# Optimization experiments

Hardware: AMD Instinct MI355X
Metric: run time of the kernel (lower is better)

## Reference

```python
import jax, jax.numpy as jnp
import numpy as np

KS = 5          # kernel_size
D = 2           # spatial dim
DX = 0.01       # region kernel spacing
SCALE = 1.0
NX, NY = 32, 32
N = NX * NY


def _region_kernel():
    # gaussians.region_kernel: KS x KS grid of offsets spaced DX, centered at 0
    off = (jnp.arange(KS, dtype=jnp.float32) - (KS - 1) / 2.0) * DX
    gx, gy = jnp.meshgrid(off, off, indexing='ij')
    return jnp.stack([gx, gy], -1).reshape(-1, D)  # (KS*KS, 2)


def _build_cov(scaling, transform):
    # Cholesky-style parameterization: L lower-triangular with diag=scaling,
    # off-diag=transform; cov = L @ L^T (d=2 closed form)
    s0, s1 = scaling[:, 0], scaling[:, 1]
    t = transform[:, 0]
    c00 = s0 * s0
    c01 = s0 * t
    c11 = t * t + s1 * s1
    return jnp.stack([jnp.stack([c00, c01], -1), jnp.stack([c01, c11], -1)], -2)


def _inv2x2(c):
    det = c[:, 0, 0] * c[:, 1, 1] - c[:, 0, 1] * c[:, 1, 0]
    inv = jnp.stack([jnp.stack([c[:, 1, 1], -c[:, 0, 1]], -1),
                     jnp.stack([-c[:, 1, 0], c[:, 0, 0]], -1)], -2)
    return inv / det[:, None, None]


def setup_inputs() -> dict:
    key = jax.random.key(0)
    ks = jax.random.split(key, 20)
    # Gaussian state: grid means as in __init__
    tx = jnp.linspace(-1.0, 1.0, NX) * SCALE
    ty = jnp.linspace(-1.0, 1.0, NY) * SCALE
    gx, gy = jnp.meshgrid(tx, ty, indexing='ij')
    means = jnp.stack([gx, gy], -1).reshape(-1, D).astype(jnp.float32)
    u = 0.1 * jax.random.normal(ks[0], (N, 1), jnp.float32)
    scaling = jnp.exp(-4.5 + 0.2 * jax.random.normal(ks[1], (N, D), jnp.float32)) * SCALE
    transform = 0.002 * jax.random.normal(ks[2], (N, 1), jnp.float32)
    opacities = 2.0 + 0.1 * jax.random.normal(ks[3], (N,), jnp.float32)
    # network weights (4 heads share the first 3 layer shapes)
    convW = 0.05 * jax.random.normal(ks[4], (4, 50, 3, KS, KS), jnp.float32)
    convb = 0.01 * jax.random.normal(ks[5], (4, 50), jnp.float32)
    embW = 0.3 * jax.random.normal(ks[6], (4, 7, 30), jnp.float32)
    embb = 0.01 * jax.random.normal(ks[7], (4, 30), jnp.float32)
    l1W = 0.1 * jax.random.normal(ks[8], (4, 80, 80), jnp.float32)
    l1b = 0.01 * jax.random.normal(ks[9], (4, 80), jnp.float32)
    outW_sol = 0.1 * jax.random.normal(ks[10], (80, 1), jnp.float32)
    outb_sol = 0.01 * jax.random.normal(ks[11], (1,), jnp.float32)
    outW_trans = 0.1 * jax.random.normal(ks[12], (80, 2), jnp.float32)
    outb_trans = 0.01 * jax.random.normal(ks[13], (2,), jnp.float32)
    outW_scale = 0.1 * jax.random.normal(ks[14], (80, 2), jnp.float32)
    outb_scale = 0.01 * jax.random.normal(ks[15], (2,), jnp.float32)
    outW_tform = 0.1 * jax.random.normal(ks[16], (80, 1), jnp.float32)
    outb_tform = 0.01 * jax.random.normal(ks[17], (1,), jnp.float32)
    return {"means": means, "u": u, "scaling": scaling, "transform": transform,
            "opacities": opacities, "convW": convW, "convb": convb,
            "embW": embW, "embb": embb, "l1W": l1W, "l1b": l1b,
            "outW_sol": outW_sol, "outb_sol": outb_sol,
            "outW_trans": outW_trans, "outb_trans": outb_trans,
            "outW_scale": outW_scale, "outb_scale": outb_scale,
            "outW_tform": outW_tform, "outb_tform": outb_tform}


def reference(means, u, scaling, transform, opacities, convW, convb, embW, embb,
              l1W, l1b, outW_sol, outb_sol, outW_trans, outb_trans,
              outW_scale, outb_scale, outW_tform, outb_tform):
    n = means.shape[0]
    cov = _build_cov(scaling, transform)          # (N,2,2)
    conics = _inv2x2(cov)                         # (N,2,2)

    # --- sampling (torch.no_grad block in original) ---
    kern = _region_kernel()                                        # (25,2)
    samples = (means[:, None, :] + kern[None]).reshape(-1, D)      # (M,2), M=N*25
    bc = jnp.all(jnp.abs(samples) < SCALE, -1).astype(means.dtype)[:, None]
    alpha = jax.nn.sigmoid(opacities)                              # (N,)
    diff = samples[:, None, :] - means[None, :, :]                 # (M,N,2)
    Cq = jnp.einsum('nij,mnj->mni', conics, diff)                  # (M,N,2)
    G = jnp.exp(-0.5 * jnp.einsum('mni,mni->mn', diff, Cq)) * alpha[None, :]  # (M,N)
    u_s = G @ u                                                    # (M,1)
    # DIFFUSION pde_rhs = trace of laplacian: sum_n G * (|C q|^2 - tr(C)) * u_n
    trC = conics[:, 0, 0] + conics[:, 1, 1]
    lap = jnp.einsum('mn,mn,nc->mc', G, (Cq ** 2).sum(-1) - trC[None, :], u)  # (M,1)
    in_samples = jax.lax.stop_gradient(jnp.concatenate([u_s, lap, bc], -1))   # (M,3)

    # (N, 25, 3) -> (N, 3, 5, 5)
    img = in_samples.reshape(n, KS * KS, -1).transpose(0, 2, 1).reshape(n, -1, KS, KS)
    in_params = jnp.concatenate([means, u, scaling, transform, opacities[:, None]], -1)  # (N,7)

    # 4 Networks: conv(5x5 -> 1x1, 50ch) + param embed(7->30) + MLP(80->80->out)
    y = jnp.tanh(jnp.einsum('ncij,kocij->kno', img, convW) + convb[:, None, :])   # (4,N,50)
    e = jnp.tanh(jnp.einsum('nf,kfg->kng', in_params, embW) + embb[:, None, :])   # (4,N,30)
    h = jnp.tanh(jnp.einsum('knf,kfg->kng', jnp.concatenate([y, e], -1), l1W)
                 + l1b[:, None, :])                                               # (4,N,80)

    deltas = h[0] @ outW_sol + outb_sol          # (N,1)
    translation = h[1] @ outW_trans + outb_trans # (N,2)
    dscale = h[2] @ outW_scale + outb_scale      # (N,2)
    dtransform = h[3] @ outW_tform + outb_tform  # (N,1)

    u_new = u + deltas
    means_new = means + translation
    scaling_new = scaling * jnp.exp(dscale)
    transform_new = transform + dtransform
    cov_new = _build_cov(scaling_new, transform_new)
    return (u_new, means_new, scaling_new, transform_new, cov_new)
```

## Files before the change

kernel.cpp:

```cpp
#include <hip/hip_runtime.h>
#include <hip/hip_bf16.h>


#define NG 1024

__device__ __forceinline__ float tanh_fast(float x) {
    return 1.0f - 2.0f / (__expf(2.0f * x) + 1.0f);
}

__global__ __launch_bounds__(256) void k_fused(
    const float* __restrict__ means, const float* __restrict__ u,
    const float* __restrict__ scal, const float* __restrict__ trans,
    const float* __restrict__ opac,
    const float* __restrict__ convW, const float* __restrict__ convb,
    const float* __restrict__ embW,  const float* __restrict__ embb,
    const float* __restrict__ l1W,   const float* __restrict__ l1b,
    const float* __restrict__ oWs,  const float* __restrict__ obs,
    const float* __restrict__ oWt,  const float* __restrict__ obt,
    const float* __restrict__ oWsc, const float* __restrict__ obsc,
    const float* __restrict__ oWtf, const float* __restrict__ obtf,
    float* __restrict__ out)
{
    __shared__ float gcomp[NG * 8];
    __shared__ float pus[2][2][32];
    __shared__ float plap[2][2][32];
    __shared__ float simg[2][80];
    __shared__ float hin[2][4][80];
    __shared__ float hv[2][4][80];
    __shared__ float semb[840];
    __shared__ float sembb[120];
    __shared__ float shead[480];
    __shared__ float sheadb[6];
    __shared__ int   cnt;

    const int t  = threadIdx.x;
    const int n0 = blockIdx.x * 2;

    const float mx0 = means[2*n0],   my0 = means[2*n0+1];
    const float mx1 = means[2*n0+2], my1 = means[2*n0+3];
    const float uu0 = u[n0],     uu1 = u[n0+1];
    const float sc00 = scal[2*n0],   sc01 = scal[2*n0+1];
    const float sc10 = scal[2*n0+2], sc11 = scal[2*n0+3];
    const float tr0 = trans[n0], tr1 = trans[n0+1];
    const float op0 = opac[n0],  op1 = opac[n0+1];

    float wcv[75];
    {
        const float* w = convW + (size_t)(t < 200 ? t : 0) * 75;
        #pragma unroll
        for (int j = 0; j < 75; ++j) wcv[j] = w[j];
    }
    float w1[80];
    {
        int k = t / 80, g = t - (t / 80) * 80;
        const float* w = l1W + (size_t)(k * 80) * 80 + g;
        #pragma unroll
        for (int f = 0; f < 80; ++f) w1[f] = w[f * 80];
    }
    float bcv  = (t < 200) ? convb[t] : 0.0f;
    float b1   = l1b[t];
    float b1k3 = l1b[256 + (t & 63)];

    for (int i = t; i < 840; i += 256) semb[i] = embW[i];
    if (t < 120) sembb[t] = embb[t];
    for (int i = t; i < 480; i += 256) {
        float v = (i < 80) ? oWs[i] : (i < 240) ? oWt[i - 80]
                : (i < 400) ? oWsc[i - 240] : oWtf[i - 400];
        shead[i] = v;
    }
    if (t < 6) sheadb[t] = (t == 0) ? obs[0] : (t < 3) ? obt[t-1]
                         : (t < 5) ? obsc[t-3] : obtf[0];

    const float bxmin = fminf(mx0, mx1) - 0.02f, bxmax = fmaxf(mx0, mx1) + 0.02f;
    const float bymin = fminf(my0, my1) - 0.02f, bymax = fmaxf(my0, my1) + 0.02f;

    if (t == 0) cnt = 0;
    __syncthreads();
    for (int g = t; g < NG; g += 256) {
        float gmx = means[2*g], gmy = means[2*g+1];
        float s0  = scal[2*g],  s1  = scal[2*g+1];
        float tt  = trans[g];
        float c00 = s0*s0, c01 = s0*tt, c11 = tt*tt + s1*s1;
        float r2  = 100.0f * (c00 + c11);
        float ddx = fmaxf(fmaxf(bxmin - gmx, gmx - bxmax), 0.0f);
        float ddy = fmaxf(fmaxf(bymin - gmy, gmy - bymax), 0.0f);
        if (ddx*ddx + ddy*ddy <= r2) {
            float idet = 1.0f / (c00*c11 - c01*c01);
            float A = c11*idet, B = -c01*idet, C = c00*idet;
            float alpha = 1.0f / (1.0f + __expf(-opac[g]));
            int slot = atomicAdd(&cnt, 1);
            float4* dst = (float4*)(gcomp + slot*8);
            dst[0] = make_float4(gmx, gmy, A, B);
            dst[1] = make_float4(C, A + C, alpha * u[g], 0.0f);
        }
    }
    __syncthreads();
    const int nsurv = cnt;

    {
        int w = t >> 6, lane = t & 63;
        int l = w >> 1;
        int hc = ((w & 1) << 1) | (lane >> 5);
        int s  = lane & 31; if (s > 24) s = 24;
        int si = s / 5, sj = s - si * 5;
        float gx = l ? mx1 : mx0, gy = l ? my1 : my0;
        float sx = gx + (float)(si - 2) * 0.01f;
        float sy = gy + (float)(sj - 2) * 0.01f;
        float us = 0.0f, lp = 0.0f;
        #pragma unroll 2
        for (int i = hc; i < nsurv; i += 4) {
            float4 a = *(const float4*)(gcomp + i*8);
            float4 b = *(const float4*)(gcomp + i*8 + 4);
            float dx = sx - a.x, dy = sy - a.y;
            float Cq0 = a.z*dx + a.w*dy;
            float Cq1 = a.w*dx + b.x*dy;
            float q   = dx*Cq0 + dy*Cq1;
            float e   = __expf(-0.5f*q) * b.z;
            us += e;
            lp += e * (Cq0*Cq0 + Cq1*Cq1 - b.y);
        }
        us += __shfl_down(us, 32);
        lp += __shfl_down(lp, 32);
        if ((lane & 31) == s && lane < 32) {
            pus[l][w & 1][s] = us; plap[l][w & 1][s] = lp;
        }
    }
    __syncthreads();

    if (t < 50) {
        int l = t / 25, s = t - l * 25;
        float us = pus[l][0][s] + pus[l][1][s];
        float lp = plap[l][0][s] + plap[l][1][s];
        int si = s / 5, sj = s - si * 5;
        float gx = l ? mx1 : mx0, gy = l ? my1 : my0;
        float sx = gx + (float)(si - 2) * 0.01f;
        float sy = gy + (float)(sj - 2) * 0.01f;
        simg[l][s]      = us;
        simg[l][25 + s] = lp;
        simg[l][50 + s] = (fabsf(sx) < 1.0f && fabsf(sy) < 1.0f) ? 1.0f : 0.0f;
    }
    __syncthreads();

    if (t < 200) {
        float a0 = bcv, a1 = bcv;
        #pragma unroll
        for (int j = 0; j < 75; ++j) {
            a0 += simg[0][j] * wcv[j];
            a1 += simg[1][j] * wcv[j];
        }
        int k = t / 50, o = t - k * 50;
        hin[0][k][o] = tanh_fast(a0);
        hin[1][k][o] = tanh_fast(a1);
    } else {
        for (int idx = t - 200; idx < 240; idx += 56) {
            int l = idx / 120, rem = idx - l * 120;
            int k = rem / 30, g = rem - k * 30;
            float acc = sembb[k * 30 + g];
            #pragma unroll
            for (int f = 0; f < 7; ++f) {
                float in0, in1;
                switch (f) {
                    case 0: in0 = mx0;  in1 = mx1;  break;
                    case 1: in0 = my0;  in1 = my1;  break;
                    case 2: in0 = uu0;  in1 = uu1;  break;
                    case 3: in0 = sc00; in1 = sc10; break;
                    case 4: in0 = sc01; in1 = sc11; break;
                    case 5: in0 = tr0;  in1 = tr1;  break;
                    default: in0 = op0; in1 = op1;  break;
                }
                acc += (l ? in1 : in0) * semb[(k*7 + f)*30 + g];
            }
            hin[l][k][50 + g] = tanh_fast(acc);
        }
    }
    __syncthreads();

    {
        int k = t / 80, g = t - (t / 80) * 80;
        float a0 = b1, a1 = b1;
        #pragma unroll
        for (int f = 0; f < 80; ++f) {
            a0 += hin[0][k][f] * w1[f];
            a1 += hin[1][k][f] * w1[f];
        }
        hv[0][k][g] = tanh_fast(a0);
        hv[1][k][g] = tanh_fast(a1);
    }
    if (t < 64) {
        int g = 16 + t;
        float a0 = b1k3, a1 = b1k3;
        #pragma unroll 8
        for (int f = 0; f < 80; ++f) {
            float w = l1W[(3*80 + f)*80 + g];
            a0 += hin[0][3][f] * w;
            a1 += hin[1][3][f] * w;
        }
        hv[0][3][g] = tanh_fast(a0);
        hv[1][3][g] = tanh_fast(a1);
    }
    __syncthreads();

    if (t < 64) {
        int l = (t / 6) & 1, t6 = t % 6;
        int k, base, stride, j;
        if (t6 == 0)      { k = 0; base = 0;   stride = 1; j = 0; }
        else if (t6 < 3)  { k = 1; base = 80;  stride = 2; j = t6 - 1; }
        else if (t6 < 5)  { k = 2; base = 240; stride = 2; j = t6 - 3; }
        else              { k = 3; base = 400; stride = 1; j = 0; }
        float acc = sheadb[t6];
        #pragma unroll 8
        for (int f = 0; f < 80; ++f)
            acc += hv[l][k][f] * shead[base + f * stride + j];

        int sb = (t / 6) * 6;
        float o0 = __shfl(acc, sb + 0);
        float o1 = __shfl(acc, sb + 1);
        float o2 = __shfl(acc, sb + 2);
        float o3 = __shfl(acc, sb + 3);
        float o4 = __shfl(acc, sb + 4);
        float o5 = __shfl(acc, sb + 5);

        if (t == 0 || t == 6) {
            int n = n0 + (t / 6);
            float uu = t ? uu1 : uu0;
            float s0 = t ? sc10 : sc00, s1 = t ? sc11 : sc01;
            float tr = t ? tr1 : tr0;
            float u_new = uu + o0;
            float mxn = (t ? mx1 : mx0) + o1;
            float myn = (t ? my1 : my0) + o2;
            float s0n = s0 * __expf(o3);
            float s1n = s1 * __expf(o4);
            float tn  = tr + o5;
            float c00 = s0n*s0n, c01 = s0n*tn, c11 = tn*tn + s1n*s1n;
            out[n]              = u_new;
            out[1024 + 2*n]     = mxn;
            out[1024 + 2*n + 1] = myn;
            out[3072 + 2*n]     = s0n;
            out[3072 + 2*n + 1] = s1n;
            out[5120 + n]       = tn;
            out[6144 + 4*n]     = c00;
            out[6144 + 4*n + 1] = c01;
            out[6144 + 4*n + 2] = c01;
            out[6144 + 4*n + 3] = c11;
        }
    }
}

extern "C" void kernel_launch(void* const* d_in, const int* in_sizes, int n_in,
                              void* d_out, int out_size, void* d_ws, size_t ws_size,
                              hipStream_t stream)
{
    k_fused<<<dim3(NG / 2), dim3(256), 0, stream>>>(
        (const float*)d_in[0],  (const float*)d_in[1],  (const float*)d_in[2],
        (const float*)d_in[3],  (const float*)d_in[4],  (const float*)d_in[5],
        (const float*)d_in[6],  (const float*)d_in[7],  (const float*)d_in[8],
        (const float*)d_in[9],  (const float*)d_in[10], (const float*)d_in[11],
        (const float*)d_in[12], (const float*)d_in[13], (const float*)d_in[14],
        (const float*)d_in[15], (const float*)d_in[16], (const float*)d_in[17],
        (const float*)d_in[18], (float*)d_out);
}
```

Baseline: 105.2 us.

## Process four Gaussians per block with float4-packed activations to amortize weight loads

Each block now handles four Gaussians instead of two, so the per-block weight loads (conv and l1 weights into registers, embedding and head weights into shared memory) and the culling pass are shared across more outputs. Intermediate activations are stored as float4 interleaved across the four Gaussians, so each weight register feeds four FMAs per shared load. This halves the grid to 256 blocks, which may reduce occupancy across the many CUs. The enlarged bounding box may also let more neighbours survive culling, and each sample now loops over half as many parallel partitions.

Result: slower. 108.7 us (+3.3%).

```diff
diff --git a/kernel.cpp b/kernel.cpp
--- a/kernel.cpp
+++ b/kernel.cpp
@@ -3,6 +3,7 @@
 
 
 #define NG 1024
+#define GPB 4
 
 __device__ __forceinline__ float tanh_fast(float x) {
     return 1.0f - 2.0f / (__expf(2.0f * x) + 1.0f);
@@ -21,12 +22,13 @@
     const float* __restrict__ oWtf, const float* __restrict__ obtf,
     float* __restrict__ out)
 {
-    __shared__ float gcomp[NG * 8];
-    __shared__ float pus[2][2][32];
-    __shared__ float plap[2][2][32];
-    __shared__ float simg[2][80];
-    __shared__ float hin[2][4][80];
-    __shared__ float hv[2][4][80];
+    __shared__ __align__(16) float gcomp[NG * 8];
+    __shared__ float pus[GPB][32];
+    __shared__ float plap[GPB][32];
+    __shared__ float4 simgv[80];
+    __shared__ float4 hinv[4][80];
+    __shared__ float4 hvv[4 * 81];
+    __shared__ float sparams[GPB][8];
     __shared__ float semb[840];
     __shared__ float sembb[120];
     __shared__ float shead[480];
@@ -34,15 +36,28 @@
     __shared__ int   cnt;
 
     const int t  = threadIdx.x;
-    const int n0 = blockIdx.x * 2;
-
-    const float mx0 = means[2*n0],   my0 = means[2*n0+1];
-    const float mx1 = means[2*n0+2], my1 = means[2*n0+3];
-    const float uu0 = u[n0],     uu1 = u[n0+1];
-    const float sc00 = scal[2*n0],   sc01 = scal[2*n0+1];
-    const float sc10 = scal[2*n0+2], sc11 = scal[2*n0+3];
-    const float tr0 = trans[n0], tr1 = trans[n0+1];
-    const float op0 = opac[n0],  op1 = opac[n0+1];
+    const int n0 = blockIdx.x * GPB;
+
+    const float m0x = means[2*n0+0], m0y = means[2*n0+1];
+    const float m1x = means[2*n0+2], m1y = means[2*n0+3];
+    const float m2x = means[2*n0+4], m2y = means[2*n0+5];
+    const float m3x = means[2*n0+6], m3y = means[2*n0+7];
+
+    if (t < 28) {
+        int l = t / 7, f = t - l * 7;
+        int n = n0 + l;
+        float v;
+        switch (f) {
+            case 0: v = means[2*n];   break;
+            case 1: v = means[2*n+1]; break;
+            case 2: v = u[n];         break;
+            case 3: v = scal[2*n];    break;
+            case 4: v = scal[2*n+1];  break;
+            case 5: v = trans[n];     break;
+            default: v = opac[n];     break;
+        }
+        sparams[l][f] = v;
+    }
 
     float wcv[75];
     {
@@ -71,8 +86,10 @@
     if (t < 6) sheadb[t] = (t == 0) ? obs[0] : (t < 3) ? obt[t-1]
                          : (t < 5) ? obsc[t-3] : obtf[0];
 
-    const float bxmin = fminf(mx0, mx1) - 0.02f, bxmax = fmaxf(mx0, mx1) + 0.02f;
-    const float bymin = fminf(my0, my1) - 0.02f, bymax = fmaxf(my0, my1) + 0.02f;
+    const float bxmin = fminf(fminf(m0x, m1x), fminf(m2x, m3x)) - 0.02f;
+    const float bxmax = fmaxf(fmaxf(m0x, m1x), fmaxf(m2x, m3x)) + 0.02f;
+    const float bymin = fminf(fminf(m0y, m1y), fminf(m2y, m3y)) - 0.02f;
+    const float bymax = fmaxf(fmaxf(m0y, m1y), fmaxf(m2y, m3y)) + 0.02f;
 
     if (t == 0) cnt = 0;
     __syncthreads();
@@ -99,16 +116,16 @@
 
     {
         int w = t >> 6, lane = t & 63;
-        int l = w >> 1;
-        int hc = ((w & 1) << 1) | (lane >> 5);
-        int s  = lane & 31; if (s > 24) s = 24;
+        int h = lane >> 5;
+        int s = lane & 31; if (s > 24) s = 24;
         int si = s / 5, sj = s - si * 5;
-        float gx = l ? mx1 : mx0, gy = l ? my1 : my0;
+        float gx = (w == 0) ? m0x : (w == 1) ? m1x : (w == 2) ? m2x : m3x;
+        float gy = (w == 0) ? m0y : (w == 1) ? m1y : (w == 2) ? m2y : m3y;
         float sx = gx + (float)(si - 2) * 0.01f;
         float sy = gy + (float)(sj - 2) * 0.01f;
         float us = 0.0f, lp = 0.0f;
         #pragma unroll 2
-        for (int i = hc; i < nsurv; i += 4) {
+        for (int i = h; i < nsurv; i += 2) {
             float4 a = *(const float4*)(gcomp + i*8);
             float4 b = *(const float4*)(gcomp + i*8 + 4);
             float dx = sx - a.x, dy = sy - a.y;
@@ -121,98 +138,99 @@
         }
         us += __shfl_down(us, 32);
         lp += __shfl_down(lp, 32);
-        if ((lane & 31) == s && lane < 32) {
-            pus[l][w & 1][s] = us; plap[l][w & 1][s] = lp;
-        }
-    }
-    __syncthreads();
-
-    if (t < 50) {
+        if (lane < 32 && (lane & 31) == s) {
+            pus[w][s] = us; plap[w][s] = lp;
+        }
+    }
+    __syncthreads();
+
+    if (t < 100) {
         int l = t / 25, s = t - l * 25;
-        float us = pus[l][0][s] + pus[l][1][s];
-        float lp = plap[l][0][s] + plap[l][1][s];
+        float us = pus[l][s];
+        float lp = plap[l][s];
         int si = s / 5, sj = s - si * 5;
-        float gx = l ? mx1 : mx0, gy = l ? my1 : my0;
+        float gx = (l == 0) ? m0x : (l == 1) ? m1x : (l == 2) ? m2x : m3x;
+        float gy = (l == 0) ? m0y : (l == 1) ? m1y : (l == 2) ? m2y : m3y;
         float sx = gx + (float)(si - 2) * 0.01f;
         float sy = gy + (float)(sj - 2) * 0.01f;
-        simg[l][s]      = us;
-        simg[l][25 + s] = lp;
-        simg[l][50 + s] = (fabsf(sx) < 1.0f && fabsf(sy) < 1.0f) ? 1.0f : 0.0f;
+        float* sg = (float*)simgv;
+        sg[(s)*4 + l]      = us;
+        sg[(25 + s)*4 + l] = lp;
+        sg[(50 + s)*4 + l] = (fabsf(sx) < 1.0f && fabsf(sy) < 1.0f) ? 1.0f : 0.0f;
     }
     __syncthreads();
 
     if (t < 200) {
-        float a0 = bcv, a1 = bcv;
+        float a0 = bcv, a1 = bcv, a2 = bcv, a3 = bcv;
         #pragma unroll
         for (int j = 0; j < 75; ++j) {
-            a0 += simg[0][j] * wcv[j];
-            a1 += simg[1][j] * wcv[j];
+            float4 v = simgv[j];
+            a0 += v.x * wcv[j];
+            a1 += v.y * wcv[j];
+            a2 += v.z * wcv[j];
+            a3 += v.w * wcv[j];
         }
         int k = t / 50, o = t - k * 50;
-        hin[0][k][o] = tanh_fast(a0);
-        hin[1][k][o] = tanh_fast(a1);
+        hinv[k][o] = make_float4(tanh_fast(a0), tanh_fast(a1),
+                                 tanh_fast(a2), tanh_fast(a3));
     } else {
-        for (int idx = t - 200; idx < 240; idx += 56) {
+        for (int idx = t - 200; idx < 480; idx += 56) {
             int l = idx / 120, rem = idx - l * 120;
             int k = rem / 30, g = rem - k * 30;
             float acc = sembb[k * 30 + g];
             #pragma unroll
-            for (int f = 0; f < 7; ++f) {
-                float in0, in1;
-                switch (f) {
-                    case 0: in0 = mx0;  in1 = mx1;  break;
-                    case 1: in0 = my0;  in1 = my1;  break;
-                    case 2: in0 = uu0;  in1 = uu1;  break;
-                    case 3: in0 = sc00; in1 = sc10; break;
-                    case 4: in0 = sc01; in1 = sc11; break;
-                    case 5: in0 = tr0;  in1 = tr1;  break;
-                    default: in0 = op0; in1 = op1;  break;
-                }
-                acc += (l ? in1 : in0) * semb[(k*7 + f)*30 + g];
-            }
-            hin[l][k][50 + g] = tanh_fast(acc);
+            for (int f = 0; f < 7; ++f)
+                acc += sparams[l][f] * semb[(k*7 + f)*30 + g];
+            ((float*)hinv)[(k*80 + 50 + g)*4 + l] = tanh_fast(acc);
         }
     }
     __syncthreads();
 
     {
         int k = t / 80, g = t - (t / 80) * 80;
-        float a0 = b1, a1 = b1;
+        float a0 = b1, a1 = b1, a2 = b1, a3 = b1;
         #pragma unroll
         for (int f = 0; f < 80; ++f) {
-            a0 += hin[0][k][f] * w1[f];
-            a1 += hin[1][k][f] * w1[f];
-        }
-        hv[0][k][g] = tanh_fast(a0);
-        hv[1][k][g] = tanh_fast(a1);
+            float4 h = hinv[k][f];
+            a0 += h.x * w1[f];
+            a1 += h.y * w1[f];
+            a2 += h.z * w1[f];
+            a3 += h.w * w1[f];
+        }
+        hvv[k*81 + g] = make_float4(tanh_fast(a0), tanh_fast(a1),
+                                    tanh_fast(a2), tanh_fast(a3));
     }
     if (t < 64) {
         int g = 16 + t;
-        float a0 = b1k3, a1 = b1k3;
+        float a0 = b1k3, a1 = b1k3, a2 = b1k3, a3 = b1k3;
         #pragma unroll 8
         for (int f = 0; f < 80; ++f) {
             float w = l1W[(3*80 + f)*80 + g];
-            a0 += hin[0][3][f] * w;
-            a1 += hin[1][3][f] * w;
-        }
-        hv[0][3][g] = tanh_fast(a0);
-        hv[1][3][g] = tanh_fast(a1);
-    }
-    __syncthreads();
-
-    if (t < 64) {
-        int l = (t / 6) & 1, t6 = t % 6;
+            float4 h = hinv[3][f];
+            a0 += h.x * w;
+            a1 += h.y * w;
+            a2 += h.z * w;
+            a3 += h.w * w;
+        }
+        hvv[3*81 + g] = make_float4(tanh_fast(a0), tanh_fast(a1),
+                                    tanh_fast(a2), tanh_fast(a3));
+    }
+    __syncthreads();
+
+    if (t < 24) {
+        int l = t / 6, t6 = t - l * 6;
         int k, base, stride, j;
         if (t6 == 0)      { k = 0; base = 0;   stride = 1; j = 0; }
         else if (t6 < 3)  { k = 1; base = 80;  stride = 2; j = t6 - 1; }
         else if (t6 < 5)  { k = 2; base = 240; stride = 2; j = t6 - 3; }
         else              { k = 3; base = 400; stride = 1; j = 0; }
         float acc = sheadb[t6];
+        const float* hvf = (const float*)hvv;
         #pragma unroll 8
         for (int f = 0; f < 80; ++f)
-            acc += hv[l][k][f] * shead[base + f * stride + j];
-
-        int sb = (t / 6) * 6;
+            acc += hvf[(k*81 + f)*4 + l] * shead[base + f * stride + j];
+
+        int sb = l * 6;
         float o0 = __shfl(acc, sb + 0);
         float o1 = __shfl(acc, sb + 1);
         float o2 = __shfl(acc, sb + 2);
@@ -220,14 +238,15 @@
         float o4 = __shfl(acc, sb + 4);
         float o5 = __shfl(acc, sb + 5);
 
-        if (t == 0 || t == 6) {
-            int n = n0 + (t / 6);
-            float uu = t ? uu1 : uu0;
-            float s0 = t ? sc10 : sc00, s1 = t ? sc11 : sc01;
-            float tr = t ? tr1 : tr0;
+        if (t6 == 0) {
+            int n = n0 + l;
+            float mx = sparams[l][0], my = sparams[l][1];
+            float uu = sparams[l][2];
+            float s0 = sparams[l][3], s1 = sparams[l][4];
+            float tr = sparams[l][5];
             float u_new = uu + o0;
-            float mxn = (t ? mx1 : mx0) + o1;
-            float myn = (t ? my1 : my0) + o2;
+            float mxn = mx + o1;
+            float myn = my + o2;
             float s0n = s0 * __expf(o3);
             float s1n = s1 * __expf(o4);
             float tn  = tr + o5;
@@ -250,7 +269,7 @@
                               void* d_out, int out_size, void* d_ws, size_t ws_size,
                               hipStream_t stream)
 {
-    k_fused<<<dim3(NG / 2), dim3(256), 0, stream>>>(
+    k_fused<<<dim3(NG / GPB), dim3(256), 0, stream>>>(
         (const float*)d_in[0],  (const float*)d_in[1],  (const float*)d_in[2],
         (const float*)d_in[3],  (const float*)d_in[4],  (const float*)d_in[5],
         (const float*)d_in[6],  (const float*)d_in[7],  (const float*)d_in[8],
```

## Prefetch gaussian and head weights into registers early, pack per-point activations as float2

Applied to the files above, without the earlier changes.

Loads of all gaussian parameters and the embedding and head weights are issued as register prefetches at kernel entry, so their latency overlaps with the conv and l1 weight loads instead of sitting behind them. The pair of points' intermediate activations are stored interleaved as float2 in shared memory, so each inner-loop step does one shared load instead of two, and hv is padded to 81 entries per head. Launch bounds now request two blocks per SM, which caps register use and may cause the 155 per-thread weight registers to spill.

After: 101.5 us. -3.6%, faster.

```diff
diff --git a/kernel.cpp b/kernel.cpp
--- a/kernel.cpp
+++ b/kernel.cpp
@@ -3,12 +3,13 @@
 
 
 #define NG 1024
+#define GPB 2
 
 __device__ __forceinline__ float tanh_fast(float x) {
     return 1.0f - 2.0f / (__expf(2.0f * x) + 1.0f);
 }
 
-__global__ __launch_bounds__(256) void k_fused(
+__global__ __launch_bounds__(256, 2) void k_fused(
     const float* __restrict__ means, const float* __restrict__ u,
     const float* __restrict__ scal, const float* __restrict__ trans,
     const float* __restrict__ opac,
@@ -21,12 +22,12 @@
     const float* __restrict__ oWtf, const float* __restrict__ obtf,
     float* __restrict__ out)
 {
-    __shared__ float gcomp[NG * 8];
+    __shared__ __align__(16) float gcomp[NG * 8];
     __shared__ float pus[2][2][32];
     __shared__ float plap[2][2][32];
-    __shared__ float simg[2][80];
-    __shared__ float hin[2][4][80];
-    __shared__ float hv[2][4][80];
+    __shared__ float2 simgv[80];
+    __shared__ float2 hinv[4][80];
+    __shared__ float2 hvv[4 * 81];
     __shared__ float semb[840];
     __shared__ float sembb[120];
     __shared__ float shead[480];
@@ -34,7 +35,31 @@
     __shared__ int   cnt;
 
     const int t  = threadIdx.x;
-    const int n0 = blockIdx.x * 2;
+    const int n0 = blockIdx.x * GPB;
+
+    float2 gm[4], gs[4];
+    float  gt[4], go[4], gu[4];
+    #pragma unroll
+    for (int i = 0; i < 4; ++i) {
+        int g = t + 256 * i;
+        gm[i] = *(const float2*)(means + 2 * g);
+        gs[i] = *(const float2*)(scal  + 2 * g);
+        gt[i] = trans[g];
+        go[i] = opac[g];
+        gu[i] = u[g];
+    }
+
+    float se0 = embW[t];
+    float se1 = embW[256 + t];
+    float se2 = embW[512 + t];
+    float se3 = (t < 72)  ? embW[768 + t] : 0.0f;
+    float sbb = (t < 120) ? embb[t] : 0.0f;
+    float sh0 = (t < 80)  ? oWs[t] : (t < 240) ? oWt[t - 80] : oWsc[t - 240];
+    float sh1 = 0.0f;
+    if (t < 224) sh1 = (t < 144) ? oWsc[t + 16] : oWtf[t - 144];
+    float shb = 0.0f;
+    if (t < 6) shb = (t == 0) ? obs[0] : (t < 3) ? obt[t-1]
+                   : (t < 5) ? obsc[t-3] : obtf[0];
 
     const float mx0 = means[2*n0],   my0 = means[2*n0+1];
     const float mx1 = means[2*n0+2], my1 = means[2*n0+3];
@@ -61,25 +86,26 @@
     float b1   = l1b[t];
     float b1k3 = l1b[256 + (t & 63)];
 
-    for (int i = t; i < 840; i += 256) semb[i] = embW[i];
-    if (t < 120) sembb[t] = embb[t];
-    for (int i = t; i < 480; i += 256) {
-        float v = (i < 80) ? oWs[i] : (i < 240) ? oWt[i - 80]
-                : (i < 400) ? oWsc[i - 240] : oWtf[i - 400];
-        shead[i] = v;
-    }
-    if (t < 6) sheadb[t] = (t == 0) ? obs[0] : (t < 3) ? obt[t-1]
-                         : (t < 5) ? obsc[t-3] : obtf[0];
-
     const float bxmin = fminf(mx0, mx1) - 0.02f, bxmax = fmaxf(mx0, mx1) + 0.02f;
     const float bymin = fminf(my0, my1) - 0.02f, bymax = fmaxf(my0, my1) + 0.02f;
 
+    semb[t]       = se0;
+    semb[256 + t] = se1;
+    semb[512 + t] = se2;
+    if (t < 72)  semb[768 + t] = se3;
+    if (t < 120) sembb[t] = sbb;
+    shead[t] = sh0;
+    if (t < 224) shead[256 + t] = sh1;
+    if (t < 6)   sheadb[t] = shb;
+
     if (t == 0) cnt = 0;
     __syncthreads();
-    for (int g = t; g < NG; g += 256) {
-        float gmx = means[2*g], gmy = means[2*g+1];
-        float s0  = scal[2*g],  s1  = scal[2*g+1];
-        float tt  = trans[g];
+
+    #pragma unroll
+    for (int i = 0; i < 4; ++i) {
+        float gmx = gm[i].x, gmy = gm[i].y;
+        float s0  = gs[i].x, s1  = gs[i].y;
+        float tt  = gt[i];
         float c00 = s0*s0, c01 = s0*tt, c11 = tt*tt + s1*s1;
         float r2  = 100.0f * (c00 + c11);
         float ddx = fmaxf(fmaxf(bxmin - gmx, gmx - bxmax), 0.0f);
@@ -87,11 +113,11 @@
         if (ddx*ddx + ddy*ddy <= r2) {
             float idet = 1.0f / (c00*c11 - c01*c01);
             float A = c11*idet, B = -c01*idet, C = c00*idet;
-            float alpha = 1.0f / (1.0f + __expf(-opac[g]));
+            float alpha = 1.0f / (1.0f + __expf(-go[i]));
             int slot = atomicAdd(&cnt, 1);
             float4* dst = (float4*)(gcomp + slot*8);
             dst[0] = make_float4(gmx, gmy, A, B);
-            dst[1] = make_float4(C, A + C, alpha * u[g], 0.0f);
+            dst[1] = make_float4(C, A + C, alpha * gu[i], 0.0f);
         }
     }
     __syncthreads();
@@ -135,9 +161,10 @@
         float gx = l ? mx1 : mx0, gy = l ? my1 : my0;
         float sx = gx + (float)(si - 2) * 0.01f;
         float sy = gy + (float)(sj - 2) * 0.01f;
-        simg[l][s]      = us;
-        simg[l][25 + s] = lp;
-        simg[l][50 + s] = (fabsf(sx) < 1.0f && fabsf(sy) < 1.0f) ? 1.0f : 0.0f;
+        float* sg = (float*)simgv;
+        sg[(s)*2 + l]      = us;
+        sg[(25 + s)*2 + l] = lp;
+        sg[(50 + s)*2 + l] = (fabsf(sx) < 1.0f && fabsf(sy) < 1.0f) ? 1.0f : 0.0f;
     }
     __syncthreads();
 
@@ -145,12 +172,12 @@
         float a0 = bcv, a1 = bcv;
         #pragma unroll
         for (int j = 0; j < 75; ++j) {
-            a0 += simg[0][j] * wcv[j];
-            a1 += simg[1][j] * wcv[j];
+            float2 v = simgv[j];
+            a0 += v.x * wcv[j];
+            a1 += v.y * wcv[j];
         }
         int k = t / 50, o = t - k * 50;
-        hin[0][k][o] = tanh_fast(a0);
-        hin[1][k][o] = tanh_fast(a1);
+        hinv[k][o] = make_float2(tanh_fast(a0), tanh_fast(a1));
     } else {
         for (int idx = t - 200; idx < 240; idx += 56) {
             int l = idx / 120, rem = idx - l * 120;
@@ -170,7 +197,7 @@
                 }
                 acc += (l ? in1 : in0) * semb[(k*7 + f)*30 + g];
             }
-            hin[l][k][50 + g] = tanh_fast(acc);
+            ((float*)hinv)[(k*80 + 50 + g)*2 + l] = tanh_fast(acc);
         }
     }
     __syncthreads();
@@ -180,11 +207,11 @@
         float a0 = b1, a1 = b1;
         #pragma unroll
         for (int f = 0; f < 80; ++f) {
-            a0 += hin[0][k][f] * w1[f];
-            a1 += hin[1][k][f] * w1[f];
-        }
-        hv[0][k][g] = tanh_fast(a0);
-        hv[1][k][g] = tanh_fast(a1);
+            float2 h = hinv[k][f];
+            a0 += h.x * w1[f];
+            a1 += h.y * w1[f];
+        }
+        hvv[k*81 + g] = make_float2(tanh_fast(a0), tanh_fast(a1));
     }
     if (t < 64) {
         int g = 16 + t;
@@ -192,11 +219,11 @@
         #pragma unroll 8
         for (int f = 0; f < 80; ++f) {
             float w = l1W[(3*80 + f)*80 + g];
-            a0 += hin[0][3][f] * w;
-            a1 += hin[1][3][f] * w;
-        }
-        hv[0][3][g] = tanh_fast(a0);
-        hv[1][3][g] = tanh_fast(a1);
+            float2 h = hinv[3][f];
+            a0 += h.x * w;
+            a1 += h.y * w;
+        }
+        hvv[3*81 + g] = make_float2(tanh_fast(a0), tanh_fast(a1));
     }
     __syncthreads();
 
@@ -208,9 +235,10 @@
         else if (t6 < 5)  { k = 2; base = 240; stride = 2; j = t6 - 3; }
         else              { k = 3; base = 400; stride = 1; j = 0; }
         float acc = sheadb[t6];
+        const float* hvf = (const float*)hvv;
         #pragma unroll 8
         for (int f = 0; f < 80; ++f)
-            acc += hv[l][k][f] * shead[base + f * stride + j];
+            acc += hvf[(k*81 + f)*2 + l] * shead[base + f * stride + j];
 
         int sb = (t / 6) * 6;
         float o0 = __shfl(acc, sb + 0);
@@ -250,7 +278,7 @@
                               void* d_out, int out_size, void* d_ws, size_t ws_size,
                               hipStream_t stream)
 {
-    k_fused<<<dim3(NG / 2), dim3(256), 0, stream>>>(
+    k_fused<<<dim3(NG / GPB), dim3(256), 0, stream>>>(
         (const float*)d_in[0],  (const float*)d_in[1],  (const float*)d_in[2],
         (const float*)d_in[3],  (const float*)d_in[4],  (const float*)d_in[5],
         (const float*)d_in[6],  (const float*)d_in[7],  (const float*)d_in[8],
```
